# Kernel optimization log

Measured on AMD Instinct MI355X. Metric: run time of the kernel, lower is better.

## Reference

```python
import jax, jax.numpy as jnp
import numpy as np

N = 100000
E = 1600000
NEG_SLOPE = 0.2


def gat_layer(x, W, al, ar, b, src, dst):
    """DGL GATConv (no dropout, no residual, bias=True, activation=None).
    x: [N, in]; W: [in, H*D]; al, ar, b: [H, D]. Returns [N, H, D]."""
    H, D = al.shape
    feat = (x @ W).reshape(N, H, D)               # [N,H,D]
    el = jnp.sum(feat * al, axis=-1)              # [N,H]
    er = jnp.sum(feat * ar, axis=-1)              # [N,H]
    e = jax.nn.leaky_relu(el[src] + er[dst], NEG_SLOPE)  # [E,H]
    # segment softmax over incoming edges of each dst node
    emax = jax.lax.stop_gradient(jax.ops.segment_max(e, dst, num_segments=N))
    ex = jnp.exp(e - emax[dst])                   # [E,H]
    denom = jax.ops.segment_sum(ex, dst, num_segments=N)  # [N,H]
    alpha = ex / jnp.where(denom[dst] == 0, 1.0, denom[dst])  # [E,H]
    msg = feat[src] * alpha[..., None]            # [E,H,D] gather + weight
    out = jax.ops.segment_sum(msg, dst, num_segments=N)    # [N,H,D] scatter-add
    return out + b[None, :, :]


def setup_inputs() -> dict:
    key = jax.random.key(0)
    ks = jax.random.split(key, 12)
    in_size, hid, out_size, heads = 128, 32, 16, 4
    x = jax.random.normal(ks[0], (N, in_size), dtype=jnp.float32)
    src = jax.random.randint(ks[1], (E,), 0, N, dtype=jnp.int32)
    dst = jax.random.randint(ks[2], (E,), 0, N, dtype=jnp.int32)
    W1 = jax.random.normal(ks[3], (in_size, heads * hid), dtype=jnp.float32) * (1.0 / np.sqrt(in_size))
    al1 = jax.random.normal(ks[4], (heads, hid), dtype=jnp.float32) * 0.1
    ar1 = jax.random.normal(ks[5], (heads, hid), dtype=jnp.float32) * 0.1
    b1 = jnp.zeros((heads, hid), dtype=jnp.float32)
    W2 = jax.random.normal(ks[6], (hid, out_size), dtype=jnp.float32) * (1.0 / np.sqrt(hid))
    al2 = jax.random.normal(ks[7], (1, out_size), dtype=jnp.float32) * 0.1
    ar2 = jax.random.normal(ks[8], (1, out_size), dtype=jnp.float32) * 0.1
    b2 = jnp.zeros((1, out_size), dtype=jnp.float32)
    return {"x": x, "src": src, "dst": dst, "W1": W1, "al1": al1, "ar1": ar1,
            "b1": b1, "W2": W2, "al2": al2, "ar2": ar2, "b2": b2}


def reference(x, src, dst, W1, al1, ar1, b1, W2, al2, ar2, b2):
    h = gat_layer(x, W1, al1, ar1, b1, src, dst)   # [N, heads, hid]
    h = jax.nn.relu(jnp.mean(h, axis=1))           # mean over heads + relu
    h = gat_layer(h, W2, al2, ar2, b2, src, dst)   # [N, 1, out]
    return h.reshape(N, -1)                        # flatten
```

## Files before the change

kernel.cpp:

```cpp
#include <hip/hip_runtime.h>
#include <hip/hip_bf16.h>

#define NEG_SLOPE 0.2f
#define LOG2E 1.44269504f
#define G_SHIFT 7
#define GSZ 128
#define CHUNK 4096
#define GSTRIDE 136

typedef __attribute__((ext_vector_type(8))) __bf16 bf16x8;
typedef __attribute__((ext_vector_type(4))) float f32x4;
typedef __attribute__((ext_vector_type(2))) float f32x2;

__device__ __forceinline__ unsigned short f2bf(float f) {
    unsigned u = __float_as_uint(f);
    unsigned r = (u + 0x7fffu + ((u >> 16) & 1u)) >> 16;
    return (unsigned short)r;
}
__device__ __forceinline__ float bflo(unsigned v) { return __uint_as_float(v << 16); }
__device__ __forceinline__ float bfhi(unsigned v) { return __uint_as_float(v & 0xffff0000u); }
__device__ __forceinline__ float bf2f(unsigned short v) {
    return __uint_as_float((unsigned)v << 16);
}

__global__ __launch_bounds__(256) void k1_scatter_wconv(
    const int* __restrict__ src, const int* __restrict__ dst,
    int* __restrict__ gcursor, unsigned* __restrict__ inter,
    const float* __restrict__ W, unsigned short* __restrict__ wtb,
    int NB, int E, int NCH) {
    __shared__ int hist[800];
    __shared__ int lbase[800];
    __shared__ int gbase[800];
    __shared__ unsigned stage[CHUNK];
    __shared__ unsigned short bstage[CHUNK];

    const int tid = threadIdx.x;
    if ((int)blockIdx.x >= NCH) {
        int idx = ((int)blockIdx.x - NCH) * 256 + tid;
        int c = idx >> 7, k = idx & 127;
        wtb[idx] = f2bf(W[k * 128 + c]);
        return;
    }

    const int e0 = blockIdx.x * CHUNK;
    const int cnt = min(CHUNK, E - e0);

    for (int i = tid; i < NB; i += 256) hist[i] = 0;
    __syncthreads();

    unsigned pk[16];
    int bb[16];
    unsigned short rk[16];
#pragma unroll
    for (int r = 0; r < 16; ++r) {
        int idx = tid + r * 256;
        if (idx < cnt) {
            int s = src[e0 + idx];
            int d = dst[e0 + idx];
            pk[r] = ((unsigned)s << G_SHIFT) | (unsigned)(d & (GSZ - 1));
            bb[r] = d >> G_SHIFT;
            rk[r] = (unsigned short)atomicAdd(&hist[bb[r]], 1);
        }
    }
    __syncthreads();
    if (tid < 64) {
        int carry = 0;
        for (int i = 0; i < NB; i += 64) {
            int v = (i + tid < NB) ? hist[i + tid] : 0;
            int xv = v;
            for (int o = 1; o < 64; o <<= 1) {
                int tt = __shfl_up(xv, o, 64);
                if (tid >= o) xv += tt;
            }
            if (i + tid < NB) lbase[i + tid] = carry + xv - v;
            carry += __shfl(xv, 63, 64);
        }
    }
    __syncthreads();
    for (int i = tid; i < NB; i += 256) {
        int hh = hist[i];
        gbase[i] = (hh > 0) ? (i * CHUNK + atomicAdd(&gcursor[i], hh)) : 0;
    }
    __syncthreads();
#pragma unroll
    for (int r = 0; r < 16; ++r) {
        int idx = tid + r * 256;
        if (idx < cnt) {
            int pos = lbase[bb[r]] + (int)rk[r];
            stage[pos] = pk[r];
            bstage[pos] = (unsigned short)bb[r];
        }
    }
    __syncthreads();
#pragma unroll
    for (int r = 0; r < 16; ++r) {
        int idx = tid + r * 256;
        if (idx < cnt) {
            int b = (int)bstage[idx];
            inter[gbase[b] + (idx - lbase[b])] = stage[idx];
        }
    }
}

__global__ __launch_bounds__(256) void k2_fine_gemm(
    const unsigned* __restrict__ inter, const int* __restrict__ gcursor,
    int* __restrict__ deg, int* __restrict__ rowptr, int* __restrict__ esrc,
    const float* __restrict__ x, const unsigned short* __restrict__ wtb,
    const float* __restrict__ al, const float* __restrict__ ar,
    unsigned short* __restrict__ featb, float* __restrict__ el,
    float* __restrict__ er, int N, int NB) {
    __shared__ __align__(16) unsigned short smem[2 * 128 * GSTRIDE];
    const int tid = threadIdx.x;

    if ((int)blockIdx.x < NB) {
        int* h = (int*)smem;
        int* lb = h + GSZ;
        int* redsum = lb + GSZ;
        const int b = blockIdx.x;
        const int cnt = gcursor[b];
        const unsigned* ep = inter + (size_t)b * CHUNK;

        {
            int s = 0;
            for (int i = tid; i < b; i += 256) s += gcursor[i];
            redsum[tid] = s;
            __syncthreads();
            for (int o = 128; o > 0; o >>= 1) {
                if (tid < o) redsum[tid] += redsum[tid + o];
                __syncthreads();
            }
        }
        const int base = redsum[0];

        if (tid < GSZ) h[tid] = 0;
        __syncthreads();
        for (int idx = tid; idx < cnt; idx += 256)
            atomicAdd(&h[(int)(ep[idx] & (GSZ - 1))], 1);
        __syncthreads();
        if (tid < 64) {
            int carry = 0;
            for (int i = 0; i < GSZ; i += 64) {
                int v = h[i + tid];
                int xv = v;
                for (int o = 1; o < 64; o <<= 1) {
                    int tt = __shfl_up(xv, o, 64);
                    if (tid >= o) xv += tt;
                }
                lb[i + tid] = carry + xv - v;
                carry += __shfl(xv, 63, 64);
            }
        }
        __syncthreads();
        if (tid < GSZ) {
            int node = b * GSZ + tid;
            if (node < N) {
                deg[node] = h[tid];
                rowptr[node] = base + lb[tid];
            }
            h[tid] = 0;
        }
        __syncthreads();
        int* eb = esrc + base;
        for (int idx = tid; idx < cnt; idx += 256) {
            unsigned ed = ep[idx];
            int l = (int)(ed & (GSZ - 1));
            int rk = atomicAdd(&h[l], 1);
            eb[lb[l] + rk] = (int)(ed >> G_SHIFT);
        }
        return;
    }

    unsigned short (*xs)[GSTRIDE] = (unsigned short(*)[GSTRIDE])smem;
    unsigned short (*ws)[GSTRIDE] = (unsigned short(*)[GSTRIDE])(smem + 128 * GSTRIDE);
    const int t = tid;
    const int m0 = ((int)blockIdx.x - NB) * 128;
    const int w = t >> 6;
    const int l = t & 63;
    const int lr = l & 15;
    const int lg = l >> 4;

    {
        const uint4* wv = (const uint4*)wtb;
#pragma unroll
        for (int rr = 0; rr < 8; ++rr) {
            int q = t + 256 * rr;
            int c = q >> 4, kb = q & 15;
            uint4 v = wv[q];
            *((uint4*)&ws[c][kb * 8]) = v;
        }
    }
    {
#pragma unroll
        for (int rr = 0; rr < 16; ++rr) {
            int q = t + 256 * rr;
            int row = q >> 5, c4 = q & 31;
            int gm = m0 + row;
            if (gm >= N) gm = N - 1;
            float4 v = *((const float4*)(x + (size_t)gm * 128 + c4 * 4));
            ushort4 o;
            o.x = f2bf(v.x); o.y = f2bf(v.y); o.z = f2bf(v.z); o.w = f2bf(v.w);
            *((ushort4*)&xs[row][c4 * 4]) = o;
        }
    }
    __syncthreads();

    f32x4 acc[2][8];
#pragma unroll
    for (int i = 0; i < 2; ++i)
#pragma unroll
        for (int j = 0; j < 8; ++j) acc[i][j] = (f32x4){0.f, 0.f, 0.f, 0.f};

#pragma unroll
    for (int kk = 0; kk < 4; ++kk) {
        const int k0 = kk * 32 + lg * 8;
        bf16x8 a0 = *((const bf16x8*)&xs[w * 32 + lr][k0]);
        bf16x8 a1 = *((const bf16x8*)&xs[w * 32 + 16 + lr][k0]);
#pragma unroll
        for (int nj = 0; nj < 8; ++nj) {
            bf16x8 bfr = *((const bf16x8*)&ws[nj * 16 + lr][k0]);
            acc[0][nj] = __builtin_amdgcn_mfma_f32_16x16x32_bf16(a0, bfr, acc[0][nj], 0, 0, 0);
            acc[1][nj] = __builtin_amdgcn_mfma_f32_16x16x32_bf16(a1, bfr, acc[1][nj], 0, 0, 0);
        }
    }
    __syncthreads();
#pragma unroll
    for (int mi = 0; mi < 2; ++mi)
#pragma unroll
        for (int r = 0; r < 4; ++r) {
            int row = w * 32 + mi * 16 + lg * 4 + r;
#pragma unroll
            for (int nj = 0; nj < 8; ++nj)
                xs[row][nj * 16 + lr] = f2bf(acc[mi][nj][r]);
        }
    __syncthreads();
    {
        int row = t >> 1, half = t & 1;
        int gm = m0 + row;
        if (gm < N) {
            float pl0 = 0.f, pl1 = 0.f, pr0 = 0.f, pr1 = 0.f;
            const unsigned short* xr = &xs[row][half * 64];
            uint4* outp = (uint4*)(featb + (size_t)gm * 128 + half * 64);
#pragma unroll
            for (int b8 = 0; b8 < 8; ++b8) {
                uint4 v = *((const uint4*)(xr + b8 * 8));
                int cb = half * 64 + b8 * 8;
                float4 a0 = *((const float4*)(al + cb));
                float4 a1 = *((const float4*)(al + cb + 4));
                float4 r0 = *((const float4*)(ar + cb));
                float4 r1 = *((const float4*)(ar + cb + 4));
                float f0 = bflo(v.x), f1 = bfhi(v.x), f2 = bflo(v.y), f3 = bfhi(v.y);
                float f4 = bflo(v.z), f5 = bfhi(v.z), f6 = bflo(v.w), f7 = bfhi(v.w);
                float sl = f0 * a0.x + f1 * a0.y + f2 * a0.z + f3 * a0.w
                         + f4 * a1.x + f5 * a1.y + f6 * a1.z + f7 * a1.w;
                float sr = f0 * r0.x + f1 * r0.y + f2 * r0.z + f3 * r0.w
                         + f4 * r1.x + f5 * r1.y + f6 * r1.z + f7 * r1.w;
                if (b8 < 4) { pl0 += sl; pr0 += sr; } else { pl1 += sl; pr1 += sr; }
                outp[b8] = v;
            }
            el[gm * 4 + half * 2 + 0] = pl0 * LOG2E;
            el[gm * 4 + half * 2 + 1] = pl1 * LOG2E;
            er[gm * 4 + half * 2 + 0] = pr0 * LOG2E;
            er[gm * 4 + half * 2 + 1] = pr1 * LOG2E;
        }
    }
}

__global__ __launch_bounds__(256) void pull1_kernel(
    const int* __restrict__ rowptr, const int* __restrict__ deg,
    const int* __restrict__ esrc, const float* __restrict__ el,
    const float* __restrict__ er, const unsigned short* __restrict__ featb,
    const float* __restrict__ b,
    const float* __restrict__ W2, const float* __restrict__ al2,
    const float* __restrict__ ar2, unsigned short* __restrict__ feat2b,
    float* __restrict__ el2, float* __restrict__ er2, int N) {
    int tid = blockIdx.x * 256 + threadIdx.x;
    int node = tid >> 4;
    int lane = threadIdx.x & 15;
    if (node >= N) return;
    int h = lane >> 2;
    int dq = lane & 3;
    int start = rowptr[node];
    int cnt = deg[node];
    float er_nh = er[node * 4 + h];
    const int* ep = esrc + start;
    const unsigned short* fb = featb + h * 32 + dq * 8;

    f32x2 acc2[4];
#pragma unroll
    for (int j = 0; j < 4; ++j) acc2[j] = (f32x2){0.f, 0.f};
    float sumex = 0.f;

    for (int i = 0; i < cnt; i += 16) {
        int s[16];
#pragma unroll
        for (int j = 0; j < 16; ++j) {
            int idx = i + j;
            idx = (idx < cnt) ? idx : (cnt - 1);
            s[j] = ep[idx];
        }
        uint4 u[16];
#pragma unroll
        for (int j = 0; j < 16; ++j) u[j] = *((const uint4*)(fb + (size_t)s[j] * 128));
        float e[16];
#pragma unroll
        for (int j = 0; j < 16; ++j) e[j] = el[s[j] * 4 + h];
#pragma unroll
        for (int j = 0; j < 16; ++j) {
            float v = e[j] + er_nh;
            v = fmaxf(v, NEG_SLOPE * v);
            float xx = (i + j < cnt) ? exp2f(v) : 0.f;
            sumex += xx;
            f32x2 xx2 = (f32x2){xx, xx};
            acc2[0] += xx2 * (f32x2){bflo(u[j].x), bfhi(u[j].x)};
            acc2[1] += xx2 * (f32x2){bflo(u[j].y), bfhi(u[j].y)};
            acc2[2] += xx2 * (f32x2){bflo(u[j].z), bfhi(u[j].z)};
            acc2[3] += xx2 * (f32x2){bflo(u[j].w), bfhi(u[j].w)};
        }
    }

    float inv = 1.f / ((sumex == 0.f) ? 1.f : sumex);
    float4 bb0 = *((const float4*)(b + h * 32 + dq * 8));
    float4 bb1 = *((const float4*)(b + h * 32 + dq * 8 + 4));
    float o[8];
    o[0] = acc2[0].x * inv + bb0.x; o[1] = acc2[0].y * inv + bb0.y;
    o[2] = acc2[1].x * inv + bb0.z; o[3] = acc2[1].y * inv + bb0.w;
    o[4] = acc2[2].x * inv + bb1.x; o[5] = acc2[2].y * inv + bb1.y;
    o[6] = acc2[3].x * inv + bb1.z; o[7] = acc2[3].y * inv + bb1.w;
#pragma unroll
    for (int j = 0; j < 8; ++j) {
        o[j] += __shfl_xor(o[j], 4);
        o[j] += __shfl_xor(o[j], 8);
        o[j] = fmaxf(o[j] * 0.25f, 0.f);
    }
    int c = lane;
    float fc = 0.f;
#pragma unroll
    for (int q = 0; q < 4; ++q) {
#pragma unroll
        for (int j = 0; j < 8; ++j) {
            float hv = __shfl(o[j], q, 16);
            fc += hv * W2[(q * 8 + j) * 16 + c];
        }
    }
    float pl = fc * al2[c];
    float pr = fc * ar2[c];
    pl += __shfl_xor(pl, 1); pl += __shfl_xor(pl, 2);
    pl += __shfl_xor(pl, 4); pl += __shfl_xor(pl, 8);
    pr += __shfl_xor(pr, 1); pr += __shfl_xor(pr, 2);
    pr += __shfl_xor(pr, 4); pr += __shfl_xor(pr, 8);
    feat2b[(size_t)node * 16 + c] = f2bf(fc);
    if (lane == 0) {
        el2[node] = pl * LOG2E;
        er2[node] = pr * LOG2E;
    }
}

__global__ __launch_bounds__(128) void pull2_kernel(
    const int* __restrict__ rowptr, const int* __restrict__ deg,
    const int* __restrict__ esrc, const float* __restrict__ el,
    const float* __restrict__ er, const unsigned short* __restrict__ feat2b,
    const float* __restrict__ b, float* __restrict__ outp, int N) {
    int tid = blockIdx.x * 128 + threadIdx.x;
    int node = tid >> 2;
    int d4 = threadIdx.x & 3;
    if (node >= N) return;

    int start = rowptr[node];
    int cnt = deg[node];
    float er_n = er[node];
    const int* ep = esrc + start;
    const unsigned short* fb = feat2b + d4 * 4;

    f32x2 acc01 = (f32x2){0.f, 0.f};
    f32x2 acc23 = (f32x2){0.f, 0.f};
    float sumex = 0.f;
    for (int i = 0; i < cnt; i += 16) {
        int s[16];
#pragma unroll
        for (int j = 0; j < 16; ++j) {
            int idx = i + j;
            idx = (idx < cnt) ? idx : (cnt - 1);
            s[j] = ep[idx];
        }
        ushort4 ff[16];
#pragma unroll
        for (int j = 0; j < 16; ++j) ff[j] = *((const ushort4*)(fb + (size_t)s[j] * 16));
        float ee[16];
#pragma unroll
        for (int j = 0; j < 16; ++j) ee[j] = el[s[j]];
#pragma unroll
        for (int j = 0; j < 16; ++j) {
            float v = ee[j] + er_n;
            v = fmaxf(v, NEG_SLOPE * v);
            float ex = (i + j < cnt) ? exp2f(v) : 0.f;
            sumex += ex;
            f32x2 ex2 = (f32x2){ex, ex};
            acc01 += ex2 * (f32x2){bf2f(ff[j].x), bf2f(ff[j].y)};
            acc23 += ex2 * (f32x2){bf2f(ff[j].z), bf2f(ff[j].w)};
        }
    }
    float inv = 1.f / ((sumex == 0.f) ? 1.f : sumex);
    float4 bb = *((const float4*)(b + d4 * 4));
    float4 o;
    o.x = acc01.x * inv + bb.x;
    o.y = acc01.y * inv + bb.y;
    o.z = acc23.x * inv + bb.z;
    o.w = acc23.y * inv + bb.w;
    *((float4*)(outp + (size_t)node * 16 + d4 * 4)) = o;
}

extern "C" void kernel_launch(void* const* d_in, const int* in_sizes, int n_in,
                              void* d_out, int out_size, void* d_ws, size_t ws_size,
                              hipStream_t stream) {
    const float* x   = (const float*)d_in[0];
    const int*   src = (const int*)d_in[1];
    const int*   dst = (const int*)d_in[2];
    const float* W1  = (const float*)d_in[3];
    const float* al1 = (const float*)d_in[4];
    const float* ar1 = (const float*)d_in[5];
    const float* b1  = (const float*)d_in[6];
    const float* W2  = (const float*)d_in[7];
    const float* al2 = (const float*)d_in[8];
    const float* ar2 = (const float*)d_in[9];
    const float* b2  = (const float*)d_in[10];

    const int E = in_sizes[1];
    const int N = in_sizes[0] / 128;
    const int H1 = 4, C1 = 128;
    const int D2 = 16;
    const int NB = (N + GSZ - 1) / GSZ;
    const int NCH = (E + CHUNK - 1) / CHUNK;
    const int GB = (N + 127) / 128;

    char* p = (char*)d_ws;
    auto alloc_f = [&](size_t n) { float* q = (float*)p; p += n * sizeof(float); return q; };
    auto alloc_i = [&](size_t n) { int* q = (int*)p; p += n * sizeof(int); return q; };

    unsigned short* feat1b = (unsigned short*)p; p += (size_t)N * C1 * sizeof(unsigned short);
    unsigned short* feat2b = (unsigned short*)p; p += (size_t)N * D2 * sizeof(unsigned short);
    float* el1   = alloc_f((size_t)N * H1);
    float* er1   = alloc_f((size_t)N * H1);
    float* el2   = alloc_f(N);
    float* er2   = alloc_f(N);
    int* deg     = alloc_i(N);
    int* rowptr  = alloc_i(N);
    int* esrc    = alloc_i(E);
    int* gcursor = alloc_i(NB);
    unsigned* inter = (unsigned*)alloc_i((size_t)NB * CHUNK);
    unsigned short* wtb = (unsigned short*)p; p += (size_t)128 * 128 * sizeof(unsigned short);

    const int TB = 256;

    hipMemsetAsync(gcursor, 0, (size_t)NB * sizeof(int), stream);
    k1_scatter_wconv<<<NCH + 64, TB, 0, stream>>>(
        src, dst, gcursor, inter, W1, wtb, NB, E, NCH);

    k2_fine_gemm<<<NB + GB, TB, 0, stream>>>(
        inter, gcursor, deg, rowptr, esrc,
        x, wtb, al1, ar1, feat1b, el1, er1, N, NB);

    pull1_kernel<<<(int)(((long long)N * 16 + 255) / 256), TB, 0, stream>>>(
        rowptr, deg, esrc, el1, er1, feat1b, b1,
        W2, al2, ar2, feat2b, el2, er2, N);

    pull2_kernel<<<(int)(((long long)N * 4 + 127) / 128), 128, 0, stream>>>(
        rowptr, deg, esrc, el2, er2, feat2b, b2, (float*)d_out, N);
}
```

Measured before the change: 251.6 us.

## Co-schedule coarse edge scatter with GEMM and split out fine scatter

```diff
diff --git a/kernel.cpp b/kernel.cpp
--- a/kernel.cpp
+++ b/kernel.cpp
@@ -23,149 +23,92 @@
     return __uint_as_float((unsigned)v << 16);
 }
 
-__global__ __launch_bounds__(256) void k1_scatter_wconv(
+__global__ __launch_bounds__(128) void wconv_kernel(
+    const float* __restrict__ W, unsigned short* __restrict__ wtb) {
+    int c = blockIdx.x;
+    int k = threadIdx.x;
+    wtb[c * 128 + k] = f2bf(W[k * 128 + c]);
+}
+
+__global__ __launch_bounds__(256) void k1_coarse_gemm(
     const int* __restrict__ src, const int* __restrict__ dst,
     int* __restrict__ gcursor, unsigned* __restrict__ inter,
-    const float* __restrict__ W, unsigned short* __restrict__ wtb,
-    int NB, int E, int NCH) {
-    __shared__ int hist[800];
-    __shared__ int lbase[800];
-    __shared__ int gbase[800];
-    __shared__ unsigned stage[CHUNK];
-    __shared__ unsigned short bstage[CHUNK];
-
-    const int tid = threadIdx.x;
-    if ((int)blockIdx.x >= NCH) {
-        int idx = ((int)blockIdx.x - NCH) * 256 + tid;
-        int c = idx >> 7, k = idx & 127;
-        wtb[idx] = f2bf(W[k * 128 + c]);
-        return;
-    }
-
-    const int e0 = blockIdx.x * CHUNK;
-    const int cnt = min(CHUNK, E - e0);
-
-    for (int i = tid; i < NB; i += 256) hist[i] = 0;
-    __syncthreads();
-
-    unsigned pk[16];
-    int bb[16];
-    unsigned short rk[16];
-#pragma unroll
-    for (int r = 0; r < 16; ++r) {
-        int idx = tid + r * 256;
-        if (idx < cnt) {
-            int s = src[e0 + idx];
-            int d = dst[e0 + idx];
-            pk[r] = ((unsigned)s << G_SHIFT) | (unsigned)(d & (GSZ - 1));
-            bb[r] = d >> G_SHIFT;
-            rk[r] = (unsigned short)atomicAdd(&hist[bb[r]], 1);
-        }
-    }
-    __syncthreads();
-    if (tid < 64) {
-        int carry = 0;
-        for (int i = 0; i < NB; i += 64) {
-            int v = (i + tid < NB) ? hist[i + tid] : 0;
-            int xv = v;
-            for (int o = 1; o < 64; o <<= 1) {
-                int tt = __shfl_up(xv, o, 64);
-                if (tid >= o) xv += tt;
-            }
-            if (i + tid < NB) lbase[i + tid] = carry + xv - v;
-            carry += __shfl(xv, 63, 64);
-        }
-    }
-    __syncthreads();
-    for (int i = tid; i < NB; i += 256) {
-        int hh = hist[i];
-        gbase[i] = (hh > 0) ? (i * CHUNK + atomicAdd(&gcursor[i], hh)) : 0;
-    }
-    __syncthreads();
-#pragma unroll
-    for (int r = 0; r < 16; ++r) {
-        int idx = tid + r * 256;
-        if (idx < cnt) {
-            int pos = lbase[bb[r]] + (int)rk[r];
-            stage[pos] = pk[r];
-            bstage[pos] = (unsigned short)bb[r];
-        }
-    }
-    __syncthreads();
-#pragma unroll
-    for (int r = 0; r < 16; ++r) {
-        int idx = tid + r * 256;
-        if (idx < cnt) {
-            int b = (int)bstage[idx];
-            inter[gbase[b] + (idx - lbase[b])] = stage[idx];
-        }
-    }
-}
-
-__global__ __launch_bounds__(256) void k2_fine_gemm(
-    const unsigned* __restrict__ inter, const int* __restrict__ gcursor,
-    int* __restrict__ deg, int* __restrict__ rowptr, int* __restrict__ esrc,
     const float* __restrict__ x, const unsigned short* __restrict__ wtb,
     const float* __restrict__ al, const float* __restrict__ ar,
     unsigned short* __restrict__ featb, float* __restrict__ el,
-    float* __restrict__ er, int N, int NB) {
+    float* __restrict__ er,
+    int N, int E, int NB, int NCH, int GB) {
     __shared__ __align__(16) unsigned short smem[2 * 128 * GSTRIDE];
     const int tid = threadIdx.x;
-
-    if ((int)blockIdx.x < NB) {
-        int* h = (int*)smem;
-        int* lb = h + GSZ;
-        int* redsum = lb + GSZ;
-        const int b = blockIdx.x;
-        const int cnt = gcursor[b];
-        const unsigned* ep = inter + (size_t)b * CHUNK;
-
-        {
-            int s = 0;
-            for (int i = tid; i < b; i += 256) s += gcursor[i];
-            redsum[tid] = s;
-            __syncthreads();
-            for (int o = 128; o > 0; o >>= 1) {
-                if (tid < o) redsum[tid] += redsum[tid + o];
-                __syncthreads();
-            }
-        }
-        const int base = redsum[0];
-
-        if (tid < GSZ) h[tid] = 0;
-        __syncthreads();
-        for (int idx = tid; idx < cnt; idx += 256)
-            atomicAdd(&h[(int)(ep[idx] & (GSZ - 1))], 1);
+    const int bid = (int)blockIdx.x;
+    const long long tot = (long long)NCH + GB;
+    const int cb  = (int)(((long long)bid * NCH) / tot);
+    const int cb1 = (int)(((long long)(bid + 1) * NCH) / tot);
+
+    if (cb1 > cb) {
+        int* hist = (int*)smem;
+        int* lbase = hist + 800;
+        int* gbase = lbase + 800;
+        unsigned* stage = (unsigned*)(gbase + 800);
+        unsigned short* bstage = (unsigned short*)(stage + CHUNK);
+
+        const int e0 = cb * CHUNK;
+        const int cnt = min(CHUNK, E - e0);
+
+        for (int i = tid; i < NB; i += 256) hist[i] = 0;
+        __syncthreads();
+
+        unsigned pk[16];
+        int bb[16];
+        unsigned short rk[16];
+#pragma unroll
+        for (int r = 0; r < 16; ++r) {
+            int idx = tid + r * 256;
+            if (idx < cnt) {
+                int s = src[e0 + idx];
+                int d = dst[e0 + idx];
+                pk[r] = ((unsigned)s << G_SHIFT) | (unsigned)(d & (GSZ - 1));
+                bb[r] = d >> G_SHIFT;
+                rk[r] = (unsigned short)atomicAdd(&hist[bb[r]], 1);
+            }
+        }
         __syncthreads();
         if (tid < 64) {
             int carry = 0;
-            for (int i = 0; i < GSZ; i += 64) {
-                int v = h[i + tid];
+            for (int i = 0; i < NB; i += 64) {
+                int v = (i + tid < NB) ? hist[i + tid] : 0;
                 int xv = v;
                 for (int o = 1; o < 64; o <<= 1) {
                     int tt = __shfl_up(xv, o, 64);
                     if (tid >= o) xv += tt;
                 }
-                lb[i + tid] = carry + xv - v;
+                if (i + tid < NB) lbase[i + tid] = carry + xv - v;
                 carry += __shfl(xv, 63, 64);
             }
         }
         __syncthreads();
-        if (tid < GSZ) {
-            int node = b * GSZ + tid;
-            if (node < N) {
-                deg[node] = h[tid];
-                rowptr[node] = base + lb[tid];
-            }
-            h[tid] = 0;
-        }
-        __syncthreads();
-        int* eb = esrc + base;
-        for (int idx = tid; idx < cnt; idx += 256) {
-            unsigned ed = ep[idx];
-            int l = (int)(ed & (GSZ - 1));
-            int rk = atomicAdd(&h[l], 1);
-            eb[lb[l] + rk] = (int)(ed >> G_SHIFT);
+        for (int i = tid; i < NB; i += 256) {
+            int hh = hist[i];
+            gbase[i] = (hh > 0) ? (i * CHUNK + atomicAdd(&gcursor[i], hh)) : 0;
+        }
+        __syncthreads();
+#pragma unroll
+        for (int r = 0; r < 16; ++r) {
+            int idx = tid + r * 256;
+            if (idx < cnt) {
+                int pos = lbase[bb[r]] + (int)rk[r];
+                stage[pos] = pk[r];
+                bstage[pos] = (unsigned short)bb[r];
+            }
+        }
+        __syncthreads();
+#pragma unroll
+        for (int r = 0; r < 16; ++r) {
+            int idx = tid + r * 256;
+            if (idx < cnt) {
+                int b = (int)bstage[idx];
+                inter[gbase[b] + (idx - lbase[b])] = stage[idx];
+            }
         }
         return;
     }
@@ -173,7 +116,7 @@
     unsigned short (*xs)[GSTRIDE] = (unsigned short(*)[GSTRIDE])smem;
     unsigned short (*ws)[GSTRIDE] = (unsigned short(*)[GSTRIDE])(smem + 128 * GSTRIDE);
     const int t = tid;
-    const int m0 = ((int)blockIdx.x - NB) * 128;
+    const int m0 = (bid - cb) * 128;
     const int w = t >> 6;
     const int l = t & 63;
     const int lr = l & 15;
@@ -243,11 +186,11 @@
 #pragma unroll
             for (int b8 = 0; b8 < 8; ++b8) {
                 uint4 v = *((const uint4*)(xr + b8 * 8));
-                int cb = half * 64 + b8 * 8;
-                float4 a0 = *((const float4*)(al + cb));
-                float4 a1 = *((const float4*)(al + cb + 4));
-                float4 r0 = *((const float4*)(ar + cb));
-                float4 r1 = *((const float4*)(ar + cb + 4));
+                int cbase = half * 64 + b8 * 8;
+                float4 a0 = *((const float4*)(al + cbase));
+                float4 a1 = *((const float4*)(al + cbase + 4));
+                float4 r0 = *((const float4*)(ar + cbase));
+                float4 r1 = *((const float4*)(ar + cbase + 4));
                 float f0 = bflo(v.x), f1 = bfhi(v.x), f2 = bflo(v.y), f3 = bfhi(v.y);
                 float f4 = bflo(v.z), f5 = bfhi(v.z), f6 = bflo(v.w), f7 = bfhi(v.w);
                 float sl = f0 * a0.x + f1 * a0.y + f2 * a0.z + f3 * a0.w
@@ -262,6 +205,67 @@
             er[gm * 4 + half * 2 + 0] = pr0 * LOG2E;
             er[gm * 4 + half * 2 + 1] = pr1 * LOG2E;
         }
+    }
+}
+
+__global__ __launch_bounds__(256) void fine_scatter(
+    const unsigned* __restrict__ inter, const int* __restrict__ gcursor,
+    int* __restrict__ deg, int* __restrict__ rowptr, int* __restrict__ esrc,
+    int N, int NB) {
+    __shared__ int h[GSZ];
+    __shared__ int lb[GSZ];
+    __shared__ int redsum[256];
+    const int b = blockIdx.x;
+    const int tid = threadIdx.x;
+    const int cnt = gcursor[b];
+    const unsigned* ep = inter + (size_t)b * CHUNK;
+
+    {
+        int s = 0;
+        for (int i = tid; i < b; i += 256) s += gcursor[i];
+        redsum[tid] = s;
+        __syncthreads();
+        for (int o = 128; o > 0; o >>= 1) {
+            if (tid < o) redsum[tid] += redsum[tid + o];
+            __syncthreads();
+        }
+    }
+    const int base = redsum[0];
+
+    if (tid < GSZ) h[tid] = 0;
+    __syncthreads();
+    for (int idx = tid; idx < cnt; idx += 256)
+        atomicAdd(&h[(int)(ep[idx] & (GSZ - 1))], 1);
+    __syncthreads();
+    if (tid < 64) {
+        int carry = 0;
+        for (int i = 0; i < GSZ; i += 64) {
+            int v = h[i + tid];
+            int xv = v;
+            for (int o = 1; o < 64; o <<= 1) {
+                int tt = __shfl_up(xv, o, 64);
+                if (tid >= o) xv += tt;
+            }
+            lb[i + tid] = carry + xv - v;
+            carry += __shfl(xv, 63, 64);
+        }
+    }
+    __syncthreads();
+    if (tid < GSZ) {
+        int node = b * GSZ + tid;
+        if (node < N) {
+            deg[node] = h[tid];
+            rowptr[node] = base + lb[tid];
+        }
+        h[tid] = 0;
+    }
+    __syncthreads();
+    int* eb = esrc + base;
+    for (int idx = tid; idx < cnt; idx += 256) {
+        unsigned ed = ep[idx];
+        int l = (int)(ed & (GSZ - 1));
+        int rk = atomicAdd(&h[l], 1);
+        eb[lb[l] + rk] = (int)(ed >> G_SHIFT);
     }
 }
 
@@ -374,7 +378,30 @@
     f32x2 acc01 = (f32x2){0.f, 0.f};
     f32x2 acc23 = (f32x2){0.f, 0.f};
     float sumex = 0.f;
-    for (int i = 0; i < cnt; i += 16) {
+    const int nfull = cnt & ~15;
+    int i = 0;
+    for (; i < nfull; i += 16) {
+        int s[16];
+#pragma unroll
+        for (int j = 0; j < 16; ++j) s[j] = ep[i + j];
+        ushort4 ff[16];
+#pragma unroll
+        for (int j = 0; j < 16; ++j) ff[j] = *((const ushort4*)(fb + (size_t)s[j] * 16));
+        float ee[16];
+#pragma unroll
+        for (int j = 0; j < 16; ++j) ee[j] = el[s[j]];
+#pragma unroll
+        for (int j = 0; j < 16; ++j) {
+            float v = ee[j] + er_n;
+            v = fmaxf(v, NEG_SLOPE * v);
+            float ex = exp2f(v);
+            sumex += ex;
+            f32x2 ex2 = (f32x2){ex, ex};
+            acc01 += ex2 * (f32x2){bf2f(ff[j].x), bf2f(ff[j].y)};
+            acc23 += ex2 * (f32x2){bf2f(ff[j].z), bf2f(ff[j].w)};
+        }
+    }
+    if (i < cnt) {
         int s[16];
 #pragma unroll
         for (int j = 0; j < 16; ++j) {
@@ -452,12 +479,14 @@
     const int TB = 256;
 
     hipMemsetAsync(gcursor, 0, (size_t)NB * sizeof(int), stream);
-    k1_scatter_wconv<<<NCH + 64, TB, 0, stream>>>(
-        src, dst, gcursor, inter, W1, wtb, NB, E, NCH);
-
-    k2_fine_gemm<<<NB + GB, TB, 0, stream>>>(
-        inter, gcursor, deg, rowptr, esrc,
-        x, wtb, al1, ar1, feat1b, el1, er1, N, NB);
+    wconv_kernel<<<128, 128, 0, stream>>>(W1, wtb);
+
+    k1_coarse_gemm<<<NCH + GB, TB, 0, stream>>>(
+        src, dst, gcursor, inter,
+        x, wtb, al1, ar1, feat1b, el1, er1,
+        N, E, NB, NCH, GB);
+
+    fine_scatter<<<NB, TB, 0, stream>>>(inter, gcursor, deg, rowptr, esrc, N, NB);
 
     pull1_kernel<<<(int)(((long long)N * 16 + 255) / 256), TB, 0, stream>>>(
         rowptr, deg, esrc, el1, er1, feat1b, b1,
```

New measurement: 245.4 us. 2.5% less time.
